# Optimization experiments

Hardware: AMD Instinct MI355X
Metric: run time of the kernel (lower is better)

The kernel has to match this reference:

```python
import jax, jax.numpy as jnp
import numpy as np

B, S, D_MODEL = 2, 2048, 1024
N_HEADS, D_HEAD = 16, 64
ATTN_SCALE = float(np.sqrt(D_HEAD))
IGNORE = -100000.0


def setup_inputs() -> dict:
    key = jax.random.key(0)
    ks = jax.random.split(key, 8)
    scale = 1.0 / np.sqrt(D_MODEL)
    return {
        "x": jax.random.normal(ks[0], (B, S, D_MODEL), jnp.float32),
        "pos_embed": jax.random.normal(ks[1], (B, S, D_MODEL), jnp.float32),
        "W_Q": jax.random.normal(ks[2], (N_HEADS, D_MODEL, D_HEAD), jnp.float32) * scale,
        "b_Q": jnp.zeros((N_HEADS, D_HEAD), jnp.float32),
        "W_K": jax.random.normal(ks[3], (N_HEADS, D_MODEL, D_HEAD), jnp.float32) * scale,
        "b_K": jnp.zeros((N_HEADS, D_HEAD), jnp.float32),
        "W_V": jax.random.normal(ks[4], (N_HEADS, D_MODEL, D_HEAD), jnp.float32) * scale,
        "b_V": jnp.zeros((N_HEADS, D_HEAD), jnp.float32),
        "W_O": jax.random.normal(ks[5], (N_HEADS, D_HEAD, D_MODEL), jnp.float32) * (1.0 / np.sqrt(D_HEAD)),
        "b_O": jnp.zeros((D_MODEL,), jnp.float32),
    }


def reference(x, pos_embed, W_Q, b_Q, W_K, b_K, W_V, b_V, W_O, b_O):
    # use_pos_resid=False: q,k read x+pos_embed, v reads x
    attn_input = x + pos_embed                                   # [b,p,m]
    q = jnp.einsum('bpm,imh->bpih', attn_input, W_Q) + b_Q       # [b,p,i,h]
    k = jnp.einsum('bpm,imh->bpih', attn_input, W_K) + b_K
    v = jnp.einsum('bpm,imh->bpih', x, W_V) + b_V
    # scores[b,i,p,q]: query index p attends to key index q
    scores = jnp.einsum('bpih,bqih->bipq', q, k) / ATTN_SCALE
    S_len = scores.shape[-1]
    causal = jnp.tril(jnp.ones((S_len, S_len), bool))
    scores = jnp.where(causal, scores, IGNORE)
    attn = jax.nn.softmax(scores, axis=-1)                       # [b,i,q_dst,p_src]
    z = jnp.einsum('bpih,biqp->bqih', v, attn)                   # [b,q,i,h]
    out = jnp.einsum('bqih,ihm->bqm', z, W_O) + b_O              # [b,q,m]
    return out
```

## Files before the change

### kernel.cpp

```cpp
#include <hip/hip_runtime.h>
#include <hip/hip_bf16.h>
#include <stdint.h>

typedef __hip_bfloat16 bf16;
typedef __attribute__((ext_vector_type(8))) short short8;
typedef __attribute__((ext_vector_type(4))) short short4v;
typedef __attribute__((ext_vector_type(4))) float f32x4;
typedef __attribute__((ext_vector_type(16))) float f32x16;
typedef __attribute__((ext_vector_type(4))) unsigned uint4v;
typedef __attribute__((ext_vector_type(2))) unsigned uint2v;

#define AS1 __attribute__((address_space(1)))
#define AS3 __attribute__((address_space(3)))

static constexpr int SEQ = 2048, DM = 1024, DHD = 64;
static constexpr int MROWS = 2 * SEQ;

__device__ __forceinline__ short f2b(float f) {
  __hip_bfloat16 h = __float2bfloat16(f);
  return *reinterpret_cast<short*>(&h);
}

__device__ __forceinline__ unsigned pack2(float lo, float hi) {
  float2 fv; fv.x = lo; fv.y = hi;
  union { __hip_bfloat162 h; unsigned u; } cv;
  cv.h = __float22bfloat162_rn(fv);
  return cv.u;
}

__device__ __forceinline__ float fexp2(float x) {
#if __has_builtin(__builtin_amdgcn_exp2f)
  return __builtin_amdgcn_exp2f(x);
#else
  return exp2f(x);
#endif
}

union U8 { uint4v u; short8 s; };

#define GL16(dst, ptr, off) \
  asm volatile("global_load_dwordx4 %0, %1, off offset:" #off : "=v"(dst) : "v"(ptr))
#define WAITV(n) do { asm volatile("s_waitcnt vmcnt(" #n ")"); __builtin_amdgcn_sched_barrier(0); } while (0)

__device__ __forceinline__ float xmax32(float v) {
#if __has_builtin(__builtin_amdgcn_permlane32_swap)
  uint2v r = __builtin_amdgcn_permlane32_swap(__float_as_uint(v), __float_as_uint(v), false, false);
  return fmaxf(__uint_as_float(r[0]), __uint_as_float(r[1]));
#else
  return fmaxf(v, __shfl_xor(v, 32));
#endif
}
__device__ __forceinline__ float xsum32(float v) {
#if __has_builtin(__builtin_amdgcn_permlane32_swap)
  uint2v r = __builtin_amdgcn_permlane32_swap(__float_as_uint(v), __float_as_uint(v), false, false);
  return __uint_as_float(r[0]) + __uint_as_float(r[1]);
#else
  return v + __shfl_xor(v, 32);
#endif
}

__global__ __launch_bounds__(256) void prep_inputs(const float* __restrict__ x,
                                                   const float* __restrict__ pos,
                                                   bf16* __restrict__ xb,
                                                   bf16* __restrict__ aib) {
  int i = blockIdx.x * 256 + threadIdx.x;
  const int n4 = MROWS * DM / 4;
  if (i >= n4) return;
  f32x4 xv = ((const f32x4*)x)[i];
  f32x4 pv = ((const f32x4*)pos)[i];
  short4v xo, ao;
#pragma unroll
  for (int j = 0; j < 4; ++j) {
    xo[j] = f2b(xv[j]);
    ao[j] = f2b(xv[j] + pv[j]);
  }
  ((short4v*)xb)[i] = xo;
  ((short4v*)aib)[i] = ao;
}

__global__ __launch_bounds__(256) void transpose_w(const float* __restrict__ in,
                                                   bf16* __restrict__ out, int R, int C) {
  __shared__ float t[64][65];
  int ct = blockIdx.x, rt = blockIdx.y, z = blockIdx.z;
  in += (size_t)z * R * C;
  out += (size_t)z * R * C;
  int c = threadIdx.x & 63, g = threadIdx.x >> 6;
#pragma unroll
  for (int j = 0; j < 16; ++j) {
    int r = g * 16 + j;
    t[r][c] = in[(size_t)(rt * 64 + r) * C + (ct * 64 + c)];
  }
  __syncthreads();
#pragma unroll
  for (int j = 0; j < 16; ++j) {
    int rr = g * 16 + j;
    out[(size_t)(ct * 64 + rr) * R + (rt * 64 + c)] = __float2bfloat16(t[c][rr]);
  }
}

template <int MODE, typename OutT>
__device__ __forceinline__ void gemm128_body(const bf16* __restrict__ A,
                                             const bf16* __restrict__ Bt,
                                             const float* __restrict__ bias,
                                             OutT* __restrict__ C, int mt, int nt,
                                             float scale) {
  __shared__ alignas(16) bf16 Al[128 * 32];
  __shared__ alignas(16) bf16 Bl[128 * 32];
  const int lane = threadIdx.x & 63, wv = threadIdx.x >> 6;
  const int wr = wv >> 1, wc = wv & 1;
  const bf16* Ab = A + (size_t)mt * 128 * DM;
  const bf16* Bb = Bt + (size_t)nt * 128 * DM;

  f32x4 acc[4][4];
#pragma unroll
  for (int i = 0; i < 4; ++i)
#pragma unroll
    for (int j = 0; j < 4; ++j) acc[i][j] = (f32x4){0.f, 0.f, 0.f, 0.f};

  for (int kt = 0; kt < DM / 32; ++kt) {
    int k0 = kt * 32;
#pragma unroll
    for (int c = 0; c < 2; ++c) {
      int li0 = wv * 64 + c * 256;
      int li = li0 + lane;
      int row = li >> 2, sl = li & 3;
      int gs = sl ^ ((row >> 1) & 3);
      __builtin_amdgcn_global_load_lds((const AS1 void*)(Ab + (size_t)row * DM + k0 + gs * 8),
                                       (AS3 void*)(&Al[li0 * 8]), 16, 0, 0);
    }
#pragma unroll
    for (int c = 0; c < 2; ++c) {
      int li0 = wv * 64 + c * 256;
      int li = li0 + lane;
      int row = li >> 2, sl = li & 3;
      int gs = sl ^ ((row >> 1) & 3);
      __builtin_amdgcn_global_load_lds((const AS1 void*)(Bb + (size_t)row * DM + k0 + gs * 8),
                                       (AS3 void*)(&Bl[li0 * 8]), 16, 0, 0);
    }
    __syncthreads();

    short8 af[4], bfr[4];
    const int kb = lane >> 4;
#pragma unroll
    for (int mi = 0; mi < 4; ++mi) {
      int r = wr * 64 + mi * 16 + (lane & 15);
      af[mi] = *(const short8*)(&Al[r * 32 + ((kb ^ ((r >> 1) & 3)) << 3)]);
    }
#pragma unroll
    for (int ni = 0; ni < 4; ++ni) {
      int r = wc * 64 + ni * 16 + (lane & 15);
      bfr[ni] = *(const short8*)(&Bl[r * 32 + ((kb ^ ((r >> 1) & 3)) << 3)]);
    }
#pragma unroll
    for (int mi = 0; mi < 4; ++mi)
#pragma unroll
      for (int ni = 0; ni < 4; ++ni)
        acc[mi][ni] = __builtin_amdgcn_mfma_f32_16x16x32_bf16(af[mi], bfr[ni], acc[mi][ni], 0, 0, 0);
    __syncthreads();
  }

#pragma unroll
  for (int mi = 0; mi < 4; ++mi) {
#pragma unroll
    for (int ni = 0; ni < 4; ++ni) {
      int row0 = mt * 128 + wr * 64 + mi * 16 + (lane >> 4) * 4;
      int col = nt * 128 + wc * 64 + ni * 16 + (lane & 15);
      float bv = bias[col];
      if constexpr (MODE == 1) {
#pragma unroll
        for (int j = 0; j < 4; ++j)
          C[(size_t)(row0 + j) * DM + col] = (acc[mi][ni][j] + bv) * scale;
      } else {
        int bb = row0 >> 11, s0 = row0 & 2047;
        int hh = col >> 6, d0 = col & 63;
        size_t bhb = (size_t)(bb * 16 + hh) * 131072;
        if constexpr (MODE == 3) {
          int kc = d0 >> 4, hi = (d0 >> 3) & 1, e = d0 & 7;
          int g = s0 >> 5, r0 = s0 & 31;
          size_t bbase = bhb + g * 2048 + kc * 512 + e;
#pragma unroll
          for (int j = 0; j < 4; ++j)
            ((bf16*)C)[bbase + (size_t)(r0 + j + 32 * hi) * 8] =
                __float2bfloat16((acc[mi][ni][j] + bv) * scale);
        } else {
          int dj = d0 >> 5, d32 = d0 & 31;
          int ks = s0 >> 4, hi2 = (s0 >> 3) & 1, e0 = s0 & 7;
          short4v o;
#pragma unroll
          for (int j = 0; j < 4; ++j) o[j] = f2b(acc[mi][ni][j] + bv);
          *(short4v*)((bf16*)C + bhb + dj * 65536 + ks * 512 + (size_t)(d32 + 32 * hi2) * 8 + e0) = o;
        }
      }
    }
  }
}

static constexpr float QSCALE = 0.125f * 1.4426950408889634f;

__global__ __launch_bounds__(256) void qkv_gemm(const bf16* __restrict__ aib,
                                                const bf16* __restrict__ xb,
                                                const bf16* __restrict__ wqt,
                                                const bf16* __restrict__ wkt,
                                                const bf16* __restrict__ wvt,
                                                const float* __restrict__ bq,
                                                const float* __restrict__ bk,
                                                const float* __restrict__ bv,
                                                bf16* __restrict__ FQ, bf16* __restrict__ FK,
                                                bf16* __restrict__ FV) {
  int mt = blockIdx.x & 31;
  int nt = (blockIdx.x >> 5) & 7;
  int mat = blockIdx.x >> 8;
  if (mat == 0) {
    gemm128_body<3>(aib, wqt, bq, FQ, mt, nt, QSCALE);
  } else if (mat == 1) {
    gemm128_body<3>(aib, wkt, bk, FK, mt, nt, 1.0f);
  } else {
    gemm128_body<4>(xb, wvt, bv, FV, mt, nt, 1.0f);
  }
}

__global__ __launch_bounds__(256) void o_gemm64(const bf16* __restrict__ A,
                                                const bf16* __restrict__ Bt,
                                                const float* __restrict__ bias,
                                                float* __restrict__ out) {
  __shared__ alignas(16) bf16 Al[64 * 32];
  __shared__ alignas(16) bf16 Bl[128 * 32];
  const int mt = blockIdx.x & 63, nt = blockIdx.x >> 6;
  const int lane = threadIdx.x & 63, wv = threadIdx.x >> 6;
  const int wr = wv >> 1, wc = wv & 1;
  const bf16* Ab = A + (size_t)mt * 64 * DM;
  const bf16* Bb = Bt + (size_t)nt * 128 * DM;

  f32x4 acc[2][4];
#pragma unroll
  for (int i = 0; i < 2; ++i)
#pragma unroll
    for (int j = 0; j < 4; ++j) acc[i][j] = (f32x4){0.f, 0.f, 0.f, 0.f};

  for (int kt = 0; kt < DM / 32; ++kt) {
    int k0 = kt * 32;
    {
      int li0 = wv * 64;
      int li = li0 + lane;
      int row = li >> 2, sl = li & 3;
      int gs = sl ^ ((row >> 1) & 3);
      __builtin_amdgcn_global_load_lds((const AS1 void*)(Ab + (size_t)row * DM + k0 + gs * 8),
                                       (AS3 void*)(&Al[li0 * 8]), 16, 0, 0);
    }
#pragma unroll
    for (int c = 0; c < 2; ++c) {
      int li0 = wv * 64 + c * 256;
      int li = li0 + lane;
      int row = li >> 2, sl = li & 3;
      int gs = sl ^ ((row >> 1) & 3);
      __builtin_amdgcn_global_load_lds((const AS1 void*)(Bb + (size_t)row * DM + k0 + gs * 8),
                                       (AS3 void*)(&Bl[li0 * 8]), 16, 0, 0);
    }
    __syncthreads();

    short8 af[2], bfr[4];
    const int kb = lane >> 4;
#pragma unroll
    for (int mi = 0; mi < 2; ++mi) {
      int r = wr * 32 + mi * 16 + (lane & 15);
      af[mi] = *(const short8*)(&Al[r * 32 + ((kb ^ ((r >> 1) & 3)) << 3)]);
    }
#pragma unroll
    for (int ni = 0; ni < 4; ++ni) {
      int r = wc * 64 + ni * 16 + (lane & 15);
      bfr[ni] = *(const short8*)(&Bl[r * 32 + ((kb ^ ((r >> 1) & 3)) << 3)]);
    }
#pragma unroll
    for (int mi = 0; mi < 2; ++mi)
#pragma unroll
      for (int ni = 0; ni < 4; ++ni)
        acc[mi][ni] = __builtin_amdgcn_mfma_f32_16x16x32_bf16(af[mi], bfr[ni], acc[mi][ni], 0, 0, 0);
    __syncthreads();
  }

#pragma unroll
  for (int mi = 0; mi < 2; ++mi) {
#pragma unroll
    for (int ni = 0; ni < 4; ++ni) {
      int row0 = mt * 64 + wr * 32 + mi * 16 + (lane >> 4) * 4;
      int col = nt * 128 + wc * 64 + ni * 16 + (lane & 15);
      float bv = bias[col];
#pragma unroll
      for (int j = 0; j < 4; ++j)
        out[(size_t)(row0 + j) * DM + col] = acc[mi][ni][j] + bv;
    }
  }
}

__global__ __launch_bounds__(128, 2) void flash_attn(const bf16* __restrict__ FQ,
                                                     const bf16* __restrict__ FK,
                                                     const bf16* __restrict__ FV,
                                                     bf16* __restrict__ Zb) {
  __shared__ float Zm[64][33];
  __shared__ float Ml[64], Ll[64];
  __shared__ unsigned Zl[32 * 32];

  const int lane = threadIdx.x & 63;
  const int wvi = threadIdx.x >> 6;
  const int qln = lane & 31;
  const bool hib = lane >= 32;
  const int bh = blockIdx.x & 31;
  const int wq = 63 - (blockIdx.x >> 5);
  const int bb = bh >> 4, h = bh & 15;
  const int q0 = wq * 32;
  const int nt = wq / 2 + 1;
  const int hsp = (nt + 1) >> 1;
  const int t0 = wvi ? hsp : 0;
  const int t1 = wvi ? nt : hsp;

  const size_t fb = (size_t)bh * 131072;
  const bf16* qp = FQ + fb + wq * 2048 + lane * 8;
  const bf16* kpt = FK + fb + (size_t)t0 * 4096 + lane * 8;
  const bf16* vp0 = FV + fb + (size_t)t0 * 2048 + lane * 8;
  const bf16* vp1 = vp0 + 65536;

  f32x16 zacc[2];
#pragma unroll
  for (int i = 0; i < 16; ++i) { zacc[0][i] = 0.f; zacc[1][i] = 0.f; }
  float mrun = -1e30f, lrun = 0.f;

  short8 qf[4];
  short8 kfA[2][4], kfB[2][4];

  if (t0 < t1) {
    GL16(qf[0], qp, 0); GL16(qf[1], qp, 1024); GL16(qf[2], qp, 2048); GL16(qf[3], qp, 3072);
    {
      const bf16* k1 = kpt + 2048;
      GL16(kfA[0][0], kpt, 0); GL16(kfA[0][1], kpt, 1024); GL16(kfA[0][2], kpt, 2048); GL16(kfA[0][3], kpt, 3072);
      GL16(kfA[1][0], k1, 0);  GL16(kfA[1][1], k1, 1024);  GL16(kfA[1][2], k1, 2048);  GL16(kfA[1][3], k1, 3072);
      kpt += 4096;
    }

    auto computeT = [&](short8(&kf)[2][4], short8(&kfn)[2][4], int t) {
      const int kv0 = t * 64;
      const bool pref = (t + 1 < t1);

      short8 vf[2][4];
      GL16(vf[0][0], vp0, 0); GL16(vf[0][1], vp0, 1024); GL16(vf[0][2], vp0, 2048); GL16(vf[0][3], vp0, 3072);
      GL16(vf[1][0], vp1, 0); GL16(vf[1][1], vp1, 1024); GL16(vf[1][2], vp1, 2048); GL16(vf[1][3], vp1, 3072);
      vp0 += 2048; vp1 += 2048;

      WAITV(8);

      f32x16 s[2];
#pragma unroll
      for (int i = 0; i < 16; ++i) { s[0][i] = 0.f; s[1][i] = 0.f; }
#pragma unroll
      for (int kc = 0; kc < 4; ++kc) {
        s[0] = __builtin_amdgcn_mfma_f32_32x32x16_bf16(kf[0][kc], qf[kc], s[0], 0, 0, 0);
        s[1] = __builtin_amdgcn_mfma_f32_32x32x16_bf16(kf[1][kc], qf[kc], s[1], 0, 0, 0);
      }

      if (pref) {
        const bf16* k1 = kpt + 2048;
        GL16(kfn[0][0], kpt, 0); GL16(kfn[0][1], kpt, 1024); GL16(kfn[0][2], kpt, 2048); GL16(kfn[0][3], kpt, 3072);
        GL16(kfn[1][0], k1, 0);  GL16(kfn[1][1], k1, 1024);  GL16(kfn[1][2], k1, 2048);  GL16(kfn[1][3], k1, 3072);
        kpt += 4096;
      }

      if (t == nt - 1) {
        const int qg = q0 + qln;
#pragma unroll
        for (int ni = 0; ni < 2; ++ni)
#pragma unroll
          for (int rr = 0; rr < 16; ++rr) {
            int kv = kv0 + 32 * ni + (rr & 3) + 8 * (rr >> 2) + (hib ? 4 : 0);
            if (kv > qg) s[ni][rr] = -1e30f;
          }
      }

      float t8[8];
#pragma unroll
      for (int i = 0; i < 8; ++i)
        t8[i] = fmaxf(fmaxf(s[0][i], s[0][i + 8]), fmaxf(s[1][i], s[1][i + 8]));
      float tm = fmaxf(fmaxf(fmaxf(t8[0], t8[1]), fmaxf(t8[2], t8[3])),
                       fmaxf(fmaxf(t8[4], t8[5]), fmaxf(t8[6], t8[7])));
      tm = xmax32(tm);

      if (__ballot(tm > mrun + 8.0f)) {
        float mn = fmaxf(mrun, tm);
        float al = fexp2(mrun - mn);
        mrun = mn;
        lrun *= al;
#pragma unroll
        for (int i = 0; i < 16; ++i) { zacc[0][i] *= al; zacc[1][i] *= al; }
      }

      float pacc[4] = {0.f, 0.f, 0.f, 0.f};
#pragma unroll
      for (int ni = 0; ni < 2; ++ni)
#pragma unroll
        for (int rr = 0; rr < 16; ++rr) {
          float p = fexp2(s[ni][rr] - mrun);
          s[ni][rr] = p;
          pacc[rr & 3] += p;
        }
      lrun += xsum32((pacc[0] + pacc[1]) + (pacc[2] + pacc[3]));

      unsigned su32[2][8];
#pragma unroll
      for (int ni = 0; ni < 2; ++ni)
#pragma unroll
        for (int tt = 0; tt < 8; ++tt)
          su32[ni][tt] = pack2(s[ni][2 * tt], s[ni][2 * tt + 1]);

      short8 pa[4];
#if __has_builtin(__builtin_amdgcn_permlane32_swap)
#pragma unroll
      for (int c = 0; c < 4; ++c) {
        int ni = c >> 1, b4 = 4 * (c & 1);
        uint2v r0 = __builtin_amdgcn_permlane32_swap(su32[ni][b4 + 0], su32[ni][b4 + 2], false, false);
        uint2v r1 = __builtin_amdgcn_permlane32_swap(su32[ni][b4 + 1], su32[ni][b4 + 3], false, false);
        U8 w;
        w.u[0] = r0[0]; w.u[1] = r1[0]; w.u[2] = r0[1]; w.u[3] = r1[1];
        pa[c] = w.s;
      }
#else
      unsigned X[2][8];
#pragma unroll
      for (int ni = 0; ni < 2; ++ni)
#pragma unroll
        for (int tt = 0; tt < 8; ++tt)
          X[ni][tt] = (unsigned)__shfl_xor((int)su32[ni][tt], 32);
#pragma unroll
      for (int c = 0; c < 4; ++c) {
        int ni = c >> 1, b4 = 4 * (c & 1);
        U8 w;
        w.u[0] = hib ? X[ni][b4 + 2] : su32[ni][b4 + 0];
        w.u[1] = hib ? X[ni][b4 + 3] : su32[ni][b4 + 1];
        w.u[2] = hib ? su32[ni][b4 + 2] : X[ni][b4 + 0];
        w.u[3] = hib ? su32[ni][b4 + 3] : X[ni][b4 + 1];
        pa[c] = w.s;
      }
#endif

      if (pref) { WAITV(8); } else { WAITV(0); }

#pragma unroll
      for (int c = 0; c < 4; ++c) {
        zacc[0] = __builtin_amdgcn_mfma_f32_32x32x16_bf16(vf[0][c], pa[c], zacc[0], 0, 0, 0);
        zacc[1] = __builtin_amdgcn_mfma_f32_32x32x16_bf16(vf[1][c], pa[c], zacc[1], 0, 0, 0);
      }
    };

    int t = t0;
    while (true) {
      computeT(kfA, kfB, t);
      if (++t >= t1) break;
      computeT(kfB, kfA, t);
      if (++t >= t1) break;
    }
  }

  if (wvi == 1) {
#pragma unroll
    for (int i = 0; i < 16; ++i) {
      Zm[lane][i] = zacc[0][i];
      Zm[lane][16 + i] = zacc[1][i];
    }
    Ml[lane] = mrun;
    Ll[lane] = lrun;
  }
  __syncthreads();
  if (wvi == 0) {
    float m1 = Ml[lane], l1 = Ll[lane];
    float mn = fmaxf(mrun, m1);
    float a0 = fexp2(mrun - mn);
    float a1 = fexp2(m1 - mn);
    float lm = lrun * a0 + l1 * a1;
#pragma unroll
    for (int i = 0; i < 16; ++i) {
      zacc[0][i] = zacc[0][i] * a0 + Zm[lane][i] * a1;
      zacc[1][i] = zacc[1][i] * a0 + Zm[lane][16 + i] * a1;
    }

    const float rl = 1.0f / lm;
    const int W8[8] = {0, 1, 4, 5, 8, 9, 12, 13};
#pragma unroll
    for (int dj = 0; dj < 2; ++dj)
#pragma unroll
      for (int tt = 0; tt < 8; ++tt) {
        unsigned v = pack2(zacc[dj][2 * tt] * rl, zacc[dj][2 * tt + 1] * rl);
        int x = 16 * dj + (hib ? 2 : 0) + W8[tt];
        Zl[qln * 32 + (((x >> 2) ^ (qln & 7)) << 2) + (x & 3)] = v;
      }
    asm volatile("s_waitcnt lgkmcnt(0)" ::: "memory");
    __builtin_amdgcn_sched_barrier(0);
    const size_t base = ((size_t)bb * SEQ) * DM + h * DHD;
    int q2 = lane >> 1, hf = lane & 1;
#pragma unroll
    for (int u = 0; u < 4; ++u) {
      int sl = (hf * 4 + u) ^ (q2 & 7);
      U8 w;
      w.u = *(const uint4v*)&Zl[q2 * 32 + sl * 4];
      *(short8*)(Zb + base + (size_t)(q0 + q2) * DM + hf * 32 + u * 8) = w.s;
    }
  }
}

extern "C" void kernel_launch(void* const* d_in, const int* in_sizes, int n_in,
                              void* d_out, int out_size, void* d_ws, size_t ws_size,
                              hipStream_t stream) {
  (void)in_sizes; (void)n_in; (void)out_size; (void)ws_size;
  const float* x = (const float*)d_in[0];
  const float* pos = (const float*)d_in[1];
  const float* WQ = (const float*)d_in[2];
  const float* bQ = (const float*)d_in[3];
  const float* WK = (const float*)d_in[4];
  const float* bK = (const float*)d_in[5];
  const float* WV = (const float*)d_in[6];
  const float* bV = (const float*)d_in[7];
  const float* WO = (const float*)d_in[8];
  const float* bO = (const float*)d_in[9];
  float* out = (float*)d_out;

  bf16* ws = (bf16*)d_ws;
  size_t off = 0;
  bf16* aib = ws + off; off += (size_t)MROWS * DM;
  bf16* xb  = ws + off; off += (size_t)MROWS * DM;
  bf16* wqt = ws + off; off += (size_t)DM * DM;
  bf16* wkt = ws + off; off += (size_t)DM * DM;
  bf16* wvt = ws + off; off += (size_t)DM * DM;
  bf16* wot = ws + off; off += (size_t)DM * DM;
  bf16* FQ  = ws + off; off += (size_t)MROWS * DM;
  bf16* FK  = ws + off; off += (size_t)MROWS * DM;
  bf16* FV  = ws + off; off += (size_t)MROWS * DM;
  bf16* Zb  = ws + off; off += (size_t)MROWS * DM;

  prep_inputs<<<(MROWS * DM / 4 + 255) / 256, 256, 0, stream>>>(x, pos, xb, aib);
  dim3 gq(1, 16, 16);
  transpose_w<<<gq, 256, 0, stream>>>(WQ, wqt, 1024, 64);
  transpose_w<<<gq, 256, 0, stream>>>(WK, wkt, 1024, 64);
  transpose_w<<<gq, 256, 0, stream>>>(WV, wvt, 1024, 64);
  dim3 go(16, 16, 1);
  transpose_w<<<go, 256, 0, stream>>>(WO, wot, 1024, 1024);
  qkv_gemm<<<768, 256, 0, stream>>>(aib, xb, wqt, wkt, wvt, bQ, bK, bV, FQ, FK, FV);
  flash_attn<<<2048, 128, 0, stream>>>(FQ, FK, FV, Zb);
  o_gemm64<<<512, 256, 0, stream>>>(Zb, wot, bO, out);
}
```

Before: 113.4 us.

## Split flash-attention KV range across four waves and raise MFMA priority

Each attention block now uses four waves instead of two, each handling a quarter of the causal KV tiles, and the partial softmax states are merged through enlarged shared-memory buffers. The S and PV MFMA sequences are wrapped in s_setprio to favor matrix issue. This targets load imbalance and latency in the long causal rows, at the cost of more merge work, more shared memory and fewer KV tiles per wave. Short rows may leave some waves with empty ranges.

```diff
diff --git a/kernel.cpp b/kernel.cpp
--- a/kernel.cpp
+++ b/kernel.cpp
@@ -292,12 +292,12 @@
   }
 }
 
-__global__ __launch_bounds__(128, 2) void flash_attn(const bf16* __restrict__ FQ,
+__global__ __launch_bounds__(256, 2) void flash_attn(const bf16* __restrict__ FQ,
                                                      const bf16* __restrict__ FK,
                                                      const bf16* __restrict__ FV,
                                                      bf16* __restrict__ Zb) {
-  __shared__ float Zm[64][33];
-  __shared__ float Ml[64], Ll[64];
+  __shared__ float Zm[3][64][33];
+  __shared__ float Ml[3][64], Ll[3][64];
   __shared__ unsigned Zl[32 * 32];
 
   const int lane = threadIdx.x & 63;
@@ -309,9 +309,8 @@
   const int bb = bh >> 4, h = bh & 15;
   const int q0 = wq * 32;
   const int nt = wq / 2 + 1;
-  const int hsp = (nt + 1) >> 1;
-  const int t0 = wvi ? hsp : 0;
-  const int t1 = wvi ? nt : hsp;
+  const int t0 = (wvi * nt) >> 2;
+  const int t1 = ((wvi + 1) * nt) >> 2;
 
   const size_t fb = (size_t)bh * 131072;
   const bf16* qp = FQ + fb + wq * 2048 + lane * 8;
@@ -350,11 +349,13 @@
       f32x16 s[2];
 #pragma unroll
       for (int i = 0; i < 16; ++i) { s[0][i] = 0.f; s[1][i] = 0.f; }
+      __builtin_amdgcn_s_setprio(1);
 #pragma unroll
       for (int kc = 0; kc < 4; ++kc) {
         s[0] = __builtin_amdgcn_mfma_f32_32x32x16_bf16(kf[0][kc], qf[kc], s[0], 0, 0, 0);
         s[1] = __builtin_amdgcn_mfma_f32_32x32x16_bf16(kf[1][kc], qf[kc], s[1], 0, 0, 0);
       }
+      __builtin_amdgcn_s_setprio(0);
 
       if (pref) {
         const bf16* k1 = kpt + 2048;
@@ -441,11 +442,13 @@
 
       if (pref) { WAITV(8); } else { WAITV(0); }
 
+      __builtin_amdgcn_s_setprio(1);
 #pragma unroll
       for (int c = 0; c < 4; ++c) {
         zacc[0] = __builtin_amdgcn_mfma_f32_32x32x16_bf16(vf[0][c], pa[c], zacc[0], 0, 0, 0);
         zacc[1] = __builtin_amdgcn_mfma_f32_32x32x16_bf16(vf[1][c], pa[c], zacc[1], 0, 0, 0);
       }
+      __builtin_amdgcn_s_setprio(0);
     };
 
     int t = t0;
@@ -457,26 +460,35 @@
     }
   }
 
-  if (wvi == 1) {
+  if (wvi != 0) {
 #pragma unroll
     for (int i = 0; i < 16; ++i) {
-      Zm[lane][i] = zacc[0][i];
-      Zm[lane][16 + i] = zacc[1][i];
-    }
-    Ml[lane] = mrun;
-    Ll[lane] = lrun;
+      Zm[wvi - 1][lane][i] = zacc[0][i];
+      Zm[wvi - 1][lane][16 + i] = zacc[1][i];
+    }
+    Ml[wvi - 1][lane] = mrun;
+    Ll[wvi - 1][lane] = lrun;
   }
   __syncthreads();
   if (wvi == 0) {
-    float m1 = Ml[lane], l1 = Ll[lane];
-    float mn = fmaxf(mrun, m1);
+    float mo[3], lo[3];
+#pragma unroll
+    for (int w = 0; w < 3; ++w) { mo[w] = Ml[w][lane]; lo[w] = Ll[w][lane]; }
+    float mn = fmaxf(fmaxf(mrun, mo[0]), fmaxf(mo[1], mo[2]));
     float a0 = fexp2(mrun - mn);
-    float a1 = fexp2(m1 - mn);
-    float lm = lrun * a0 + l1 * a1;
+    float aw[3];
+#pragma unroll
+    for (int w = 0; w < 3; ++w) aw[w] = fexp2(mo[w] - mn);
+    float lm = lrun * a0 + lo[0] * aw[0] + lo[1] * aw[1] + lo[2] * aw[2];
 #pragma unroll
     for (int i = 0; i < 16; ++i) {
-      zacc[0][i] = zacc[0][i] * a0 + Zm[lane][i] * a1;
-      zacc[1][i] = zacc[1][i] * a0 + Zm[lane][16 + i] * a1;
+      float z0 = zacc[0][i] * a0, z1 = zacc[1][i] * a0;
+#pragma unroll
+      for (int w = 0; w < 3; ++w) {
+        z0 += Zm[w][lane][i] * aw[w];
+        z1 += Zm[w][lane][16 + i] * aw[w];
+      }
+      zacc[0][i] = z0; zacc[1][i] = z1;
     }
 
     const float rl = 1.0f / lm;
@@ -540,6 +552,6 @@
   dim3 go(16, 16, 1);
   transpose_w<<<go, 256, 0, stream>>>(WO, wot, 1024, 1024);
   qkv_gemm<<<768, 256, 0, stream>>>(aib, xb, wqt, wkt, wvt, bQ, bK, bV, FQ, FK, FV);
-  flash_attn<<<2048, 128, 0, stream>>>(FQ, FK, FV, Zb);
+  flash_attn<<<2048, 256, 0, stream>>>(FQ, FK, FV, Zb);
   o_gemm64<<<512, 256, 0, stream>>>(Zb, wot, bO, out);
 }
```

Result: slower. 116.5 us (+2.8%).
